# Performance work log

Measured on AMD Instinct MI355X. Metric: run time of the kernel, lower is better.

The kernel has to match this reference:

```python
import jax, jax.numpy as jnp
import numpy as np

EPS = 1e-12
BETA = 0.25

def normalise(x, axis=-1):
    return x * jax.lax.rsqrt(jnp.mean(x * x, axis=axis, keepdims=True) + EPS)

def setup_inputs() -> dict:
    key = jax.random.key(0)
    ks = jax.random.split(key, 4)
    N, F, D, C = 8192, 512, 64, 8192
    return {
        "z": jax.random.normal(ks[0], (N, F), dtype=jnp.float32),
        "W_in": jax.random.normal(ks[1], (F, D), dtype=jnp.float32) * (1.0 / np.sqrt(F)),
        "b_in": jnp.zeros((D,), dtype=jnp.float32),
        "codebook": jax.random.normal(ks[2], (C, D), dtype=jnp.float32),
        "W_out": jax.random.normal(ks[3], (D, F), dtype=jnp.float32) * (1.0 / np.sqrt(D)),
        "b_out": jnp.zeros((F,), dtype=jnp.float32),
    }

def reference(z, W_in, b_in, codebook, W_out, b_out):
    sg = jax.lax.stop_gradient
    # input projection: [N, F] -> [N, D]
    zp = z @ W_in + b_in
    zn = normalise(zp)                  # [N, D]
    cn = normalise(codebook)            # [C, D]
    # squared euclidean distance via matmul expansion (same math as
    # sum((z[:,None]-c[None])**2, -1), avoids [N,C,D] materialization)
    z_sq = jnp.sum(zn * zn, axis=-1, keepdims=True)          # [N, 1]
    c_sq = jnp.sum(cn * cn, axis=-1)[None, :]                # [1, C]
    distance = z_sq + c_sq - 2.0 * (zn @ cn.T)               # [N, C]
    idxes = jnp.argmin(distance, axis=-1)                    # [N]
    codes = normalise(codebook[idxes], axis=-1)               # [N, D]
    loss = BETA * jnp.mean((sg(zn) - codes) ** 2) + jnp.mean((zn - sg(codes)) ** 2)
    codes = zn + sg(codes - zn)                               # straight-through
    out = codes @ W_out + b_out                               # [N, F]
    return (out, loss, idxes)
```

## Files before the change

kernel.cpp:

```cpp
#include <hip/hip_runtime.h>
#include <hip/hip_bf16.h>

#define N_ROWS 8192
#define F_DIM  512
#define D_DIM  64
#define C_CODES 8192

typedef __attribute__((ext_vector_type(8))) short bf16x8;
typedef __attribute__((ext_vector_type(4))) float f32x4;

__device__ __forceinline__ unsigned short rne_bf16(float x) {
  unsigned u = __float_as_uint(x);
  return (unsigned short)((u + 0x7FFFu + ((u >> 16) & 1u)) >> 16);
}
__device__ __forceinline__ float bf16_to_f(unsigned short u) {
  return __uint_as_float(((unsigned)u) << 16);
}
__device__ __forceinline__ void limb3(const float* xs, bf16x8& H, bf16x8& M, bf16x8& L) {
  #pragma unroll
  for (int j = 0; j < 8; ++j) {
    float x = xs[j];
    unsigned short h = rne_bf16(x);
    float r1 = x - bf16_to_f(h);
    unsigned short m = rne_bf16(r1);
    float r2 = r1 - bf16_to_f(m);
    unsigned short lo = rne_bf16(r2);
    H[j] = (short)h; M[j] = (short)m; L[j] = (short)lo;
  }
}

__global__ __launch_bounds__(256) void k_prep(
    const float* __restrict__ W_in, const float* __restrict__ W_out,
    const float* __restrict__ cb,
    unsigned short* __restrict__ win_sw, unsigned short* __restrict__ wout_sw,
    float* __restrict__ cn, unsigned short* __restrict__ cn_sw) {
  const int tid = threadIdx.x, w = tid >> 6, l = tid & 63;
  const int lo = l & 15, hi = l >> 4;
  const int bid = blockIdx.x;

  if (bid < 16) {
    const int task = bid * 4 + w;
    const int kc = task >> 2, cg = task & 3;
    float xs[8];
    #pragma unroll
    for (int j = 0; j < 8; ++j)
      xs[j] = W_in[(size_t)(kc * 32 + hi * 8 + j) * D_DIM + cg * 16 + lo];
    bf16x8 H, M, L;
    limb3(xs, H, M, L);
    const int fb = (kc * 4 + cg) * 3;
    unsigned short* d0 = win_sw + (size_t)(fb + 0) * 512 + l * 8;
    unsigned short* d1 = win_sw + (size_t)(fb + 1) * 512 + l * 8;
    unsigned short* d2 = win_sw + (size_t)(fb + 2) * 512 + l * 8;
    #pragma unroll
    for (int j = 0; j < 8; ++j) { d0[j] = (unsigned short)H[j]; d1[j] = (unsigned short)M[j]; d2[j] = (unsigned short)L[j]; }
  } else if (bid < 32) {
    const int task = (bid - 16) * 4 + w;
    const int cg = task >> 1, c = task & 1;
    float xs[8];
    #pragma unroll
    for (int j = 0; j < 8; ++j)
      xs[j] = W_out[(size_t)(c * 32 + hi * 8 + j) * F_DIM + cg * 16 + lo];
    bf16x8 H, M, L;
    limb3(xs, H, M, L);
    const int fb = (cg * 2 + c) * 3;
    unsigned short* d0 = wout_sw + (size_t)(fb + 0) * 512 + l * 8;
    unsigned short* d1 = wout_sw + (size_t)(fb + 1) * 512 + l * 8;
    unsigned short* d2 = wout_sw + (size_t)(fb + 2) * 512 + l * 8;
    #pragma unroll
    for (int j = 0; j < 8; ++j) { d0[j] = (unsigned short)H[j]; d1[j] = (unsigned short)M[j]; d2[j] = (unsigned short)L[j]; }
  } else {
    const int g = (bid - 32) * 4 + w;
    const int code = g * 16 + lo;
    float xs[2][8];
    float s = 0.0f;
    #pragma unroll
    for (int c = 0; c < 2; ++c) {
      const float* sp = cb + (size_t)code * D_DIM + c * 32 + hi * 8;
      float4 a = *(const float4*)sp, b = *(const float4*)(sp + 4);
      xs[c][0]=a.x; xs[c][1]=a.y; xs[c][2]=a.z; xs[c][3]=a.w;
      xs[c][4]=b.x; xs[c][5]=b.y; xs[c][6]=b.z; xs[c][7]=b.w;
      #pragma unroll
      for (int j = 0; j < 8; ++j) s += xs[c][j] * xs[c][j];
    }
    s += __shfl_xor(s, 16);
    s += __shfl_xor(s, 32);
    float inv = rsqrtf(s * (1.0f / 64.0f) + 1e-12f);
    #pragma unroll
    for (int c = 0; c < 2; ++c) {
      #pragma unroll
      for (int j = 0; j < 8; ++j) xs[c][j] *= inv;
      float* dp = cn + (size_t)code * D_DIM + c * 32 + hi * 8;
      *(float4*)dp = make_float4(xs[c][0], xs[c][1], xs[c][2], xs[c][3]);
      *(float4*)(dp + 4) = make_float4(xs[c][4], xs[c][5], xs[c][6], xs[c][7]);
      bf16x8 H, M, L;
      limb3(xs[c], H, M, L);
      const int fb = (g * 2 + c) * 3;
      unsigned short* d0 = cn_sw + (size_t)(fb + 0) * 512 + l * 8;
      unsigned short* d1 = cn_sw + (size_t)(fb + 1) * 512 + l * 8;
      unsigned short* d2 = cn_sw + (size_t)(fb + 2) * 512 + l * 8;
      #pragma unroll
      for (int j = 0; j < 8; ++j) { d0[j] = (unsigned short)H[j]; d1[j] = (unsigned short)M[j]; d2[j] = (unsigned short)L[j]; }
    }
  }
}

__global__ __launch_bounds__(256) void k_zn(
    const float* __restrict__ z, const unsigned short* __restrict__ w_in_sw,
    const float* __restrict__ b_in, float* __restrict__ zn,
    unsigned short* __restrict__ zn_sw) {
  __shared__ float red[4096];
  __shared__ float t_lds[16 * 65];
  const int tid = threadIdx.x, w = tid >> 6, l = tid & 63;
  const int lo = l & 15, hi = l >> 4;
  const int g = blockIdx.x;
  const int r0 = g * 16;
  const int kcb = w * 4;
  const bf16x8* Bptr = (const bf16x8*)w_in_sw;
  const float* zbase = z + (size_t)(r0 + lo) * F_DIM + hi * 8;

  f32x4 acc[4];
  #pragma unroll
  for (int cg = 0; cg < 4; ++cg) acc[cg] = (f32x4){0.f, 0.f, 0.f, 0.f};

  bf16x8 Bu[12], Bv[12];
  #pragma unroll
  for (int i = 0; i < 12; ++i) Bu[i] = Bptr[((size_t)kcb * 12 + i) * 64 + l];
  float4 za = *(const float4*)(zbase + kcb * 32);
  float4 zb = *(const float4*)(zbase + kcb * 32 + 4);

  #define ZMFMA(BCUR)                                                         \
    {                                                                         \
      float xs[8] = {za.x, za.y, za.z, za.w, zb.x, zb.y, zb.z, zb.w};         \
      bf16x8 Ah, Am, Al;                                                      \
      limb3(xs, Ah, Am, Al);                                                  \
      _Pragma("unroll")                                                       \
      for (int cg = 0; cg < 4; ++cg) {                                        \
        f32x4 t = acc[cg];                                                    \
        t = __builtin_amdgcn_mfma_f32_16x16x32_bf16(Ah, BCUR[cg*3+0], t, 0,0,0); \
        t = __builtin_amdgcn_mfma_f32_16x16x32_bf16(Ah, BCUR[cg*3+1], t, 0,0,0); \
        t = __builtin_amdgcn_mfma_f32_16x16x32_bf16(Am, BCUR[cg*3+0], t, 0,0,0); \
        t = __builtin_amdgcn_mfma_f32_16x16x32_bf16(Ah, BCUR[cg*3+2], t, 0,0,0); \
        t = __builtin_amdgcn_mfma_f32_16x16x32_bf16(Al, BCUR[cg*3+0], t, 0,0,0); \
        t = __builtin_amdgcn_mfma_f32_16x16x32_bf16(Am, BCUR[cg*3+1], t, 0,0,0); \
        acc[cg] = t;                                                          \
      }                                                                       \
    }

  {
    float4 na = *(const float4*)(zbase + (kcb + 1) * 32);
    float4 nb = *(const float4*)(zbase + (kcb + 1) * 32 + 4);
    #pragma unroll
    for (int i = 0; i < 12; ++i) Bv[i] = Bptr[((size_t)(kcb + 1) * 12 + i) * 64 + l];
    ZMFMA(Bu)
    za = na; zb = nb;
  }
  {
    float4 na = *(const float4*)(zbase + (kcb + 2) * 32);
    float4 nb = *(const float4*)(zbase + (kcb + 2) * 32 + 4);
    #pragma unroll
    for (int i = 0; i < 12; ++i) Bu[i] = Bptr[((size_t)(kcb + 2) * 12 + i) * 64 + l];
    ZMFMA(Bv)
    za = na; zb = nb;
  }
  {
    float4 na = *(const float4*)(zbase + (kcb + 3) * 32);
    float4 nb = *(const float4*)(zbase + (kcb + 3) * 32 + 4);
    #pragma unroll
    for (int i = 0; i < 12; ++i) Bv[i] = Bptr[((size_t)(kcb + 3) * 12 + i) * 64 + l];
    ZMFMA(Bu)
    za = na; zb = nb;
  }
  ZMFMA(Bv)
  #undef ZMFMA

  #pragma unroll
  for (int cg = 0; cg < 4; ++cg)
    #pragma unroll
    for (int r = 0; r < 4; ++r)
      red[((w * 4 + cg) * 4 + r) * 64 + l] = acc[cg][r];
  __syncthreads();

  {
    float v[4], s = 0.0f;
    #pragma unroll
    for (int cg = 0; cg < 4; ++cg) {
      float t = b_in[cg * 16 + lo];
      #pragma unroll
      for (int w2 = 0; w2 < 4; ++w2) t += red[((w2 * 4 + cg) * 4 + w) * 64 + l];
      v[cg] = t; s += t * t;
    }
    s += __shfl_xor(s, 1);
    s += __shfl_xor(s, 2);
    s += __shfl_xor(s, 4);
    s += __shfl_xor(s, 8);
    float inv = rsqrtf(s * (1.0f / 64.0f) + 1e-12f);
    #pragma unroll
    for (int cg = 0; cg < 4; ++cg)
      t_lds[(hi * 4 + w) * 65 + cg * 16 + lo] = v[cg] * inv;
  }
  __syncthreads();

  if (w < 2) {
    const int c = w;
    float xs[8];
    #pragma unroll
    for (int j = 0; j < 8; ++j) xs[j] = t_lds[lo * 65 + c * 32 + hi * 8 + j];
    float* dp = zn + (size_t)(r0 + lo) * D_DIM + c * 32 + hi * 8;
    *(float4*)dp = make_float4(xs[0], xs[1], xs[2], xs[3]);
    *(float4*)(dp + 4) = make_float4(xs[4], xs[5], xs[6], xs[7]);
    bf16x8 H, M, L;
    limb3(xs, H, M, L);
    const int fb = (g * 2 + c) * 3;
    unsigned short* d0 = zn_sw + (size_t)(fb + 0) * 512 + l * 8;
    unsigned short* d1 = zn_sw + (size_t)(fb + 1) * 512 + l * 8;
    unsigned short* d2 = zn_sw + (size_t)(fb + 2) * 512 + l * 8;
    #pragma unroll
    for (int j = 0; j < 8; ++j) { d0[j] = (unsigned short)H[j]; d1[j] = (unsigned short)M[j]; d2[j] = (unsigned short)L[j]; }
  }
}

__global__ __launch_bounds__(256, 4) void k_argmax(
    const unsigned short* __restrict__ zn_sw,
    const unsigned short* __restrict__ cn_sw,
    float* __restrict__ pval, int* __restrict__ pidx) {
  const int tid = threadIdx.x;
  const int w = tid >> 6, l = tid & 63;
  const int lo = l & 15, hi = l >> 4;
  const int gA0 = (blockIdx.x * 4 + w) * 2;
  const int gB0 = blockIdx.y * 32;
  const bf16x8* Ab = (const bf16x8*)zn_sw;
  const bf16x8* Bb = (const bf16x8*)cn_sw;

  bf16x8 A0[2][3], A1[2][3];
  #pragma unroll
  for (int c = 0; c < 2; ++c)
    #pragma unroll
    for (int m = 0; m < 3; ++m) {
      A0[c][m] = Ab[(size_t)((gA0 * 2 + c) * 3 + m) * 64 + l];
      A1[c][m] = Ab[(size_t)(((gA0 + 1) * 2 + c) * 3 + m) * 64 + l];
    }

  bf16x8 Bu[2][3], Bv[2][3];
  #pragma unroll
  for (int c = 0; c < 2; ++c)
    #pragma unroll
    for (int m = 0; m < 3; ++m)
      Bu[c][m] = Bb[(size_t)((gB0 * 2 + c) * 3 + m) * 64 + l];

  float bv[8];
  int bi[8];
  #pragma unroll
  for (int i = 0; i < 8; ++i) { bv[i] = -1e30f; bi[i] = 0; }
  int cand = blockIdx.y * 512 + lo;

  #define LOADB(dst, gB)                                                     \
    _Pragma("unroll")                                                        \
    for (int c = 0; c < 2; ++c)                                              \
      _Pragma("unroll")                                                      \
      for (int m = 0; m < 3; ++m)                                            \
        dst[c][m] = Bb[(size_t)(((gB) * 2 + c) * 3 + m) * 64 + l];

  #define COMPUTE(B)                                                          \
    {                                                                         \
      f32x4 a0 = {0.f,0.f,0.f,0.f}, a1 = {0.f,0.f,0.f,0.f};                   \
      f32x4 a2 = {0.f,0.f,0.f,0.f}, a3 = {0.f,0.f,0.f,0.f};                   \
      a0 = __builtin_amdgcn_mfma_f32_16x16x32_bf16(A0[0][0], B[0][0], a0, 0,0,0); \
      a1 = __builtin_amdgcn_mfma_f32_16x16x32_bf16(A0[1][0], B[1][0], a1, 0,0,0); \
      a2 = __builtin_amdgcn_mfma_f32_16x16x32_bf16(A1[0][0], B[0][0], a2, 0,0,0); \
      a3 = __builtin_amdgcn_mfma_f32_16x16x32_bf16(A1[1][0], B[1][0], a3, 0,0,0); \
      a0 = __builtin_amdgcn_mfma_f32_16x16x32_bf16(A0[0][0], B[0][1], a0, 0,0,0); \
      a1 = __builtin_amdgcn_mfma_f32_16x16x32_bf16(A0[1][0], B[1][1], a1, 0,0,0); \
      a2 = __builtin_amdgcn_mfma_f32_16x16x32_bf16(A1[0][0], B[0][1], a2, 0,0,0); \
      a3 = __builtin_amdgcn_mfma_f32_16x16x32_bf16(A1[1][0], B[1][1], a3, 0,0,0); \
      a0 = __builtin_amdgcn_mfma_f32_16x16x32_bf16(A0[0][1], B[0][0], a0, 0,0,0); \
      a1 = __builtin_amdgcn_mfma_f32_16x16x32_bf16(A0[1][1], B[1][0], a1, 0,0,0); \
      a2 = __builtin_amdgcn_mfma_f32_16x16x32_bf16(A1[0][1], B[0][0], a2, 0,0,0); \
      a3 = __builtin_amdgcn_mfma_f32_16x16x32_bf16(A1[1][1], B[1][0], a3, 0,0,0); \
      a0 = __builtin_amdgcn_mfma_f32_16x16x32_bf16(A0[0][0], B[0][2], a0, 0,0,0); \
      a1 = __builtin_amdgcn_mfma_f32_16x16x32_bf16(A0[1][0], B[1][2], a1, 0,0,0); \
      a2 = __builtin_amdgcn_mfma_f32_16x16x32_bf16(A1[0][0], B[0][2], a2, 0,0,0); \
      a3 = __builtin_amdgcn_mfma_f32_16x16x32_bf16(A1[1][0], B[1][2], a3, 0,0,0); \
      a0 = __builtin_amdgcn_mfma_f32_16x16x32_bf16(A0[0][2], B[0][0], a0, 0,0,0); \
      a1 = __builtin_amdgcn_mfma_f32_16x16x32_bf16(A0[1][2], B[1][0], a1, 0,0,0); \
      a2 = __builtin_amdgcn_mfma_f32_16x16x32_bf16(A1[0][2], B[0][0], a2, 0,0,0); \
      a3 = __builtin_amdgcn_mfma_f32_16x16x32_bf16(A1[1][2], B[1][0], a3, 0,0,0); \
      a0 = __builtin_amdgcn_mfma_f32_16x16x32_bf16(A0[0][1], B[0][1], a0, 0,0,0); \
      a1 = __builtin_amdgcn_mfma_f32_16x16x32_bf16(A0[1][1], B[1][1], a1, 0,0,0); \
      a2 = __builtin_amdgcn_mfma_f32_16x16x32_bf16(A1[0][1], B[0][1], a2, 0,0,0); \
      a3 = __builtin_amdgcn_mfma_f32_16x16x32_bf16(A1[1][1], B[1][1], a3, 0,0,0); \
      _Pragma("unroll")                                                       \
      for (int r = 0; r < 4; ++r) {                                           \
        float d0 = a0[r] + a1[r];                                             \
        if (d0 > bv[r]) { bv[r] = d0; bi[r] = cand; }                         \
        float d1 = a2[r] + a3[r];                                             \
        if (d1 > bv[4 + r]) { bv[4 + r] = d1; bi[4 + r] = cand; }             \
      }                                                                       \
      cand += 16;                                                             \
    }

  for (int p = 0; p < 32; p += 2) {
    LOADB(Bv, gB0 + p + 1);
    COMPUTE(Bu);
    LOADB(Bu, gB0 + p + 2);
    COMPUTE(Bv);
  }
  #undef LOADB
  #undef COMPUTE

  #pragma unroll
  for (int i = 0; i < 8; ++i) {
    float v = bv[i]; int ix = bi[i];
    #pragma unroll
    for (int m = 1; m < 16; m <<= 1) {
      float ov = __shfl_xor(v, m);
      int oi = __shfl_xor(ix, m);
      if (ov > v || (ov == v && oi < ix)) { v = ov; ix = oi; }
    }
    bv[i] = v; bi[i] = ix;
  }
  if (lo == 0) {
    int off = blockIdx.y * N_ROWS;
    int base0 = gA0 * 16 + hi * 4;
    int base1 = (gA0 + 1) * 16 + hi * 4;
    #pragma unroll
    for (int r = 0; r < 4; ++r) {
      pval[off + base0 + r] = bv[r];     pidx[off + base0 + r] = bi[r];
      pval[off + base1 + r] = bv[4 + r]; pidx[off + base1 + r] = bi[4 + r];
    }
  }
}

__global__ __launch_bounds__(256) void k_out(
    const float* __restrict__ cn, const float* __restrict__ zn,
    const float* __restrict__ pval, const int* __restrict__ pidx,
    const unsigned short* __restrict__ w_out_sw,
    const float* __restrict__ b_out, float* __restrict__ out,
    float* __restrict__ idx_f, float* __restrict__ pl) {
  const int tid = threadIdx.x, w = tid >> 6, l = tid & 63;
  const int lo = l & 15, hi = l >> 4;
  const int r0 = blockIdx.x * 16;
  const int row = r0 + lo;

  float v = pval[row];
  int ix = pidx[row];
  #pragma unroll
  for (int q = 1; q < 16; ++q) {
    float vq = pval[q * N_ROWS + row];
    int iq = pidx[q * N_ROWS + row];
    if (vq > v) { v = vq; ix = iq; }
  }
  if (w == 0 && hi == 0) idx_f[row] = (float)ix;

  bf16x8 A[2][3];
  float lp = 0.0f;
  #pragma unroll
  for (int c = 0; c < 2; ++c) {
    const float* cp = cn + (size_t)ix * D_DIM + c * 32 + hi * 8;
    const float* zp = zn + (size_t)row * D_DIM + c * 32 + hi * 8;
    float4 c0 = *(const float4*)cp, c1 = *(const float4*)(cp + 4);
    float4 z0 = *(const float4*)zp, z1 = *(const float4*)(zp + 4);
    float xs[8] = {c0.x, c0.y, c0.z, c0.w, c1.x, c1.y, c1.z, c1.w};
    float zs[8] = {z0.x, z0.y, z0.z, z0.w, z1.x, z1.y, z1.z, z1.w};
    limb3(xs, A[c][0], A[c][1], A[c][2]);
    #pragma unroll
    for (int j = 0; j < 8; ++j) { float d = xs[j] - zs[j]; lp += d * d; }
  }
  if (w == 0) {
    #pragma unroll
    for (int m = 1; m < 64; m <<= 1) lp += __shfl_xor(lp, m);
    if (l == 0) pl[blockIdx.x] = lp;
  }

  const bf16x8* Bptr = (const bf16x8*)w_out_sw;
  const int cgb = w * 8;
  bf16x8 Bu[6], Bv[6];
  #pragma unroll
  for (int i = 0; i < 6; ++i) Bu[i] = Bptr[((size_t)cgb * 6 + i) * 64 + l];

  #define OSTEP(BCUR, BNXT, CG)                                               \
    {                                                                         \
      _Pragma("unroll")                                                       \
      for (int i = 0; i < 6; ++i)                                             \
        BNXT[i] = Bptr[((size_t)((CG) + 1) * 6 + i) * 64 + l];                \
      f32x4 a0 = {0.f,0.f,0.f,0.f}, a1 = {0.f,0.f,0.f,0.f};                   \
      a0 = __builtin_amdgcn_mfma_f32_16x16x32_bf16(A[0][0], BCUR[0], a0, 0,0,0); \
      a1 = __builtin_amdgcn_mfma_f32_16x16x32_bf16(A[1][0], BCUR[3], a1, 0,0,0); \
      a0 = __builtin_amdgcn_mfma_f32_16x16x32_bf16(A[0][0], BCUR[1], a0, 0,0,0); \
      a1 = __builtin_amdgcn_mfma_f32_16x16x32_bf16(A[1][0], BCUR[4], a1, 0,0,0); \
      a0 = __builtin_amdgcn_mfma_f32_16x16x32_bf16(A[0][1], BCUR[0], a0, 0,0,0); \
      a1 = __builtin_amdgcn_mfma_f32_16x16x32_bf16(A[1][1], BCUR[3], a1, 0,0,0); \
      a0 = __builtin_amdgcn_mfma_f32_16x16x32_bf16(A[0][0], BCUR[2], a0, 0,0,0); \
      a1 = __builtin_amdgcn_mfma_f32_16x16x32_bf16(A[1][0], BCUR[5], a1, 0,0,0); \
      a0 = __builtin_amdgcn_mfma_f32_16x16x32_bf16(A[0][2], BCUR[0], a0, 0,0,0); \
      a1 = __builtin_amdgcn_mfma_f32_16x16x32_bf16(A[1][2], BCUR[3], a1, 0,0,0); \
      a0 = __builtin_amdgcn_mfma_f32_16x16x32_bf16(A[0][1], BCUR[1], a0, 0,0,0); \
      a1 = __builtin_amdgcn_mfma_f32_16x16x32_bf16(A[1][1], BCUR[4], a1, 0,0,0); \
      float bb = b_out[(CG) * 16 + lo];                                       \
      _Pragma("unroll")                                                       \
      for (int r = 0; r < 4; ++r)                                             \
        out[(size_t)(r0 + hi * 4 + r) * F_DIM + (CG) * 16 + lo] =             \
            a0[r] + a1[r] + bb;                                               \
    }

  for (int cg = cgb; cg < cgb + 8; cg += 2) {
    OSTEP(Bu, Bv, cg)
    OSTEP(Bv, Bu, cg + 1)
  }
  #undef OSTEP
}

__global__ __launch_bounds__(64) void k_loss_final(
    const float* __restrict__ pl, float* __restrict__ loss_out) {
  const int l = threadIdx.x;
  float s = 0.0f;
  #pragma unroll
  for (int i = 0; i < 8; ++i) s += pl[l + 64 * i];
  #pragma unroll
  for (int m = 1; m < 64; m <<= 1) s += __shfl_xor(s, m);
  if (l == 0) loss_out[0] = s * (1.25f / (float)(N_ROWS * D_DIM));
}

extern "C" void kernel_launch(void* const* d_in, const int* in_sizes, int n_in,
                              void* d_out, int out_size, void* d_ws, size_t ws_size,
                              hipStream_t stream) {
  const float* z        = (const float*)d_in[0];
  const float* W_in     = (const float*)d_in[1];
  const float* b_in     = (const float*)d_in[2];
  const float* codebook = (const float*)d_in[3];
  const float* W_out    = (const float*)d_in[4];
  const float* b_out    = (const float*)d_in[5];

  float* outp   = (float*)d_out;
  float* loss_f = outp + (size_t)N_ROWS * F_DIM;
  float* idx_f  = loss_f + 1;

  float* wsf = (float*)d_ws;
  float* zn_ws = wsf;
  float* cn_ws = wsf + 524288;
  unsigned short* zn_sw = (unsigned short*)(wsf + 1048576);
  unsigned short* cn_sw = (unsigned short*)(wsf + 1835008);
  unsigned short* win_sw  = (unsigned short*)(wsf + 2625536);
  unsigned short* wout_sw = (unsigned short*)(wsf + 2674688);
  float* pval_ws = wsf + 2723840;
  int*   pidx_ws = (int*)(wsf + 2854912);
  float* pl_ws   = wsf + 2985984;

  hipLaunchKernelGGL(k_prep, dim3(160), dim3(256), 0, stream,
                     W_in, W_out, codebook, win_sw, wout_sw, cn_ws, cn_sw);
  hipLaunchKernelGGL(k_zn, dim3(512), dim3(256), 0, stream,
                     z, win_sw, b_in, zn_ws, zn_sw);
  hipLaunchKernelGGL(k_argmax, dim3(64, 16), dim3(256), 0, stream,
                     zn_sw, cn_sw, pval_ws, pidx_ws);
  hipLaunchKernelGGL(k_out, dim3(512), dim3(256), 0, stream,
                     cn_ws, zn_ws, pval_ws, pidx_ws, wout_sw, b_out,
                     outp, idx_f, pl_ws);
  hipLaunchKernelGGL(k_loss_final, dim3(1), dim3(64), 0, stream,
                     pl_ws, loss_f);
}
```

Measured before the change: 153.2 us.

## Stage codebook tiles in LDS via async global_load_lds double buffering

The argmax kernel used to have every wave load the same codebook fragments from global memory into registers. Now the four waves of a block share the work: each copies its slice of the codebook tiles into LDS with global_load_lds, double buffered across 16 stages and separated by __syncthreads, and every wave then reads all fragments back from LDS. This removes the four-fold redundant global/L2 traffic for B and frees B registers, at the cost of LDS reads, block barriers and a dropped occupancy hint in launch_bounds. A possible risk is that the barrier does not wait for the async LDS load to complete, since no explicit vmcnt wait is visible.

```diff
diff --git a/kernel.cpp b/kernel.cpp
--- a/kernel.cpp
+++ b/kernel.cpp
@@ -27,6 +27,12 @@
     unsigned short lo = rne_bf16(r2);
     H[j] = (short)h; M[j] = (short)m; L[j] = (short)lo;
   }
+}
+
+typedef __attribute__((address_space(1))) const unsigned char gas_uchar;
+typedef __attribute__((address_space(3))) unsigned char las_uchar;
+__device__ __forceinline__ void gld_lds16(const void* g, void* l) {
+  __builtin_amdgcn_global_load_lds((gas_uchar*)g, (las_uchar*)l, 16, 0, 0);
 }
 
 __global__ __launch_bounds__(256) void k_prep(
@@ -219,17 +225,18 @@
   }
 }
 
-__global__ __launch_bounds__(256, 4) void k_argmax(
+__global__ __launch_bounds__(256) void k_argmax(
     const unsigned short* __restrict__ zn_sw,
     const unsigned short* __restrict__ cn_sw,
     float* __restrict__ pval, int* __restrict__ pidx) {
+  __shared__ short smem[2 * 12 * 512];
   const int tid = threadIdx.x;
   const int w = tid >> 6, l = tid & 63;
   const int lo = l & 15, hi = l >> 4;
   const int gA0 = (blockIdx.x * 4 + w) * 2;
   const int gB0 = blockIdx.y * 32;
   const bf16x8* Ab = (const bf16x8*)zn_sw;
-  const bf16x8* Bb = (const bf16x8*)cn_sw;
+  const char* Bbytes = (const char*)cn_sw;
 
   bf16x8 A0[2][3], A1[2][3];
   #pragma unroll
@@ -240,54 +247,43 @@
       A1[c][m] = Ab[(size_t)(((gA0 + 1) * 2 + c) * 3 + m) * 64 + l];
     }
 
-  bf16x8 Bu[2][3], Bv[2][3];
-  #pragma unroll
-  for (int c = 0; c < 2; ++c)
-    #pragma unroll
-    for (int m = 0; m < 3; ++m)
-      Bu[c][m] = Bb[(size_t)((gB0 * 2 + c) * 3 + m) * 64 + l];
-
   float bv[8];
   int bi[8];
   #pragma unroll
   for (int i = 0; i < 8; ++i) { bv[i] = -1e30f; bi[i] = 0; }
   int cand = blockIdx.y * 512 + lo;
 
-  #define LOADB(dst, gB)                                                     \
-    _Pragma("unroll")                                                        \
-    for (int c = 0; c < 2; ++c)                                              \
-      _Pragma("unroll")                                                      \
-      for (int m = 0; m < 3; ++m)                                            \
-        dst[c][m] = Bb[(size_t)(((gB) * 2 + c) * 3 + m) * 64 + l];
-
-  #define COMPUTE(B)                                                          \
+  #define STAGE(b, s)                                                         \
     {                                                                         \
+      const int fb = (gB0 + (s) * 2) * 6 + w * 3;                             \
+      _Pragma("unroll")                                                       \
+      for (int i = 0; i < 3; ++i)                                             \
+        gld_lds16(Bbytes + ((size_t)(fb + i) << 10) + (size_t)l * 16,         \
+                  &smem[((b) * 12 + w * 3 + i) * 512]);                       \
+    }
+
+  #define MF(A_, B_, C_) __builtin_amdgcn_mfma_f32_16x16x32_bf16(A_, B_, C_, 0, 0, 0)
+
+  #define COMPUTE(LF)                                                         \
+    {                                                                         \
+      bf16x8 Bf[6];                                                           \
+      _Pragma("unroll")                                                       \
+      for (int i = 0; i < 6; ++i)                                             \
+        Bf[i] = *(const bf16x8*)&smem[((LF) + i) * 512 + l * 8];              \
       f32x4 a0 = {0.f,0.f,0.f,0.f}, a1 = {0.f,0.f,0.f,0.f};                   \
       f32x4 a2 = {0.f,0.f,0.f,0.f}, a3 = {0.f,0.f,0.f,0.f};                   \
-      a0 = __builtin_amdgcn_mfma_f32_16x16x32_bf16(A0[0][0], B[0][0], a0, 0,0,0); \
-      a1 = __builtin_amdgcn_mfma_f32_16x16x32_bf16(A0[1][0], B[1][0], a1, 0,0,0); \
-      a2 = __builtin_amdgcn_mfma_f32_16x16x32_bf16(A1[0][0], B[0][0], a2, 0,0,0); \
-      a3 = __builtin_amdgcn_mfma_f32_16x16x32_bf16(A1[1][0], B[1][0], a3, 0,0,0); \
-      a0 = __builtin_amdgcn_mfma_f32_16x16x32_bf16(A0[0][0], B[0][1], a0, 0,0,0); \
-      a1 = __builtin_amdgcn_mfma_f32_16x16x32_bf16(A0[1][0], B[1][1], a1, 0,0,0); \
-      a2 = __builtin_amdgcn_mfma_f32_16x16x32_bf16(A1[0][0], B[0][1], a2, 0,0,0); \
-      a3 = __builtin_amdgcn_mfma_f32_16x16x32_bf16(A1[1][0], B[1][1], a3, 0,0,0); \
-      a0 = __builtin_amdgcn_mfma_f32_16x16x32_bf16(A0[0][1], B[0][0], a0, 0,0,0); \
-      a1 = __builtin_amdgcn_mfma_f32_16x16x32_bf16(A0[1][1], B[1][0], a1, 0,0,0); \
-      a2 = __builtin_amdgcn_mfma_f32_16x16x32_bf16(A1[0][1], B[0][0], a2, 0,0,0); \
-      a3 = __builtin_amdgcn_mfma_f32_16x16x32_bf16(A1[1][1], B[1][0], a3, 0,0,0); \
-      a0 = __builtin_amdgcn_mfma_f32_16x16x32_bf16(A0[0][0], B[0][2], a0, 0,0,0); \
-      a1 = __builtin_amdgcn_mfma_f32_16x16x32_bf16(A0[1][0], B[1][2], a1, 0,0,0); \
-      a2 = __builtin_amdgcn_mfma_f32_16x16x32_bf16(A1[0][0], B[0][2], a2, 0,0,0); \
-      a3 = __builtin_amdgcn_mfma_f32_16x16x32_bf16(A1[1][0], B[1][2], a3, 0,0,0); \
-      a0 = __builtin_amdgcn_mfma_f32_16x16x32_bf16(A0[0][2], B[0][0], a0, 0,0,0); \
-      a1 = __builtin_amdgcn_mfma_f32_16x16x32_bf16(A0[1][2], B[1][0], a1, 0,0,0); \
-      a2 = __builtin_amdgcn_mfma_f32_16x16x32_bf16(A1[0][2], B[0][0], a2, 0,0,0); \
-      a3 = __builtin_amdgcn_mfma_f32_16x16x32_bf16(A1[1][2], B[1][0], a3, 0,0,0); \
-      a0 = __builtin_amdgcn_mfma_f32_16x16x32_bf16(A0[0][1], B[0][1], a0, 0,0,0); \
-      a1 = __builtin_amdgcn_mfma_f32_16x16x32_bf16(A0[1][1], B[1][1], a1, 0,0,0); \
-      a2 = __builtin_amdgcn_mfma_f32_16x16x32_bf16(A1[0][1], B[0][1], a2, 0,0,0); \
-      a3 = __builtin_amdgcn_mfma_f32_16x16x32_bf16(A1[1][1], B[1][1], a3, 0,0,0); \
+      a0 = MF(A0[0][0], Bf[0], a0); a1 = MF(A0[1][0], Bf[3], a1);             \
+      a2 = MF(A1[0][0], Bf[0], a2); a3 = MF(A1[1][0], Bf[3], a3);             \
+      a0 = MF(A0[0][0], Bf[1], a0); a1 = MF(A0[1][0], Bf[4], a1);             \
+      a2 = MF(A1[0][0], Bf[1], a2); a3 = MF(A1[1][0], Bf[4], a3);             \
+      a0 = MF(A0[0][1], Bf[0], a0); a1 = MF(A0[1][1], Bf[3], a1);             \
+      a2 = MF(A1[0][1], Bf[0], a2); a3 = MF(A1[1][1], Bf[3], a3);             \
+      a0 = MF(A0[0][0], Bf[2], a0); a1 = MF(A0[1][0], Bf[5], a1);             \
+      a2 = MF(A1[0][0], Bf[2], a2); a3 = MF(A1[1][0], Bf[5], a3);             \
+      a0 = MF(A0[0][2], Bf[0], a0); a1 = MF(A0[1][2], Bf[3], a1);             \
+      a2 = MF(A1[0][2], Bf[0], a2); a3 = MF(A1[1][2], Bf[3], a3);             \
+      a0 = MF(A0[0][1], Bf[1], a0); a1 = MF(A0[1][1], Bf[4], a1);             \
+      a2 = MF(A1[0][1], Bf[1], a2); a3 = MF(A1[1][1], Bf[4], a3);             \
       _Pragma("unroll")                                                       \
       for (int r = 0; r < 4; ++r) {                                           \
         float d0 = a0[r] + a1[r];                                             \
@@ -298,14 +294,19 @@
       cand += 16;                                                             \
     }
 
-  for (int p = 0; p < 32; p += 2) {
-    LOADB(Bv, gB0 + p + 1);
-    COMPUTE(Bu);
-    LOADB(Bu, gB0 + p + 2);
-    COMPUTE(Bv);
-  }
-  #undef LOADB
+  STAGE(0, 0)
+  __syncthreads();
+  int cur = 0;
+  for (int s = 0; s < 16; ++s) {
+    if (s < 15) STAGE(cur ^ 1, s + 1)
+    COMPUTE(cur * 12 + 0)
+    COMPUTE(cur * 12 + 6)
+    __syncthreads();
+    cur ^= 1;
+  }
+  #undef STAGE
   #undef COMPUTE
+  #undef MF
 
   #pragma unroll
   for (int i = 0; i < 8; ++i) {
```

Measured after the change: 141.6 us. 1.08x faster.
